# Optimization experiments

Hardware: AMD Instinct MI355X
Metric: run time of the kernel (lower is better)

Reference implementation:

```python
import jax, jax.numpy as jnp
import numpy as np

DIM, NH, WS, SS = 192, 6, 8, 4
B, H, W = 4, 192, 192
MID = max(DIM // 16, 4)
N = WS * WS
HD = DIM // NH
SCALE = HD ** -0.5

def _rel_index():
    coords = np.stack(np.meshgrid(np.arange(WS), np.arange(WS), indexing='ij')).reshape(2, -1)
    rel = (coords[:, :, None] - coords[:, None, :]).transpose(1, 2, 0)
    rel[..., 0] += WS - 1
    rel[..., 1] += WS - 1
    rel[..., 0] *= 2 * WS - 1
    return rel.sum(-1)  # (N, N)

REL_IDX = jnp.asarray(_rel_index())

def _shift_mask():
    img = np.zeros((1, H, W, 1), np.float32)
    sl = (slice(0, -WS), slice(-WS, -SS), slice(-SS, None))
    cnt = 0
    for hs in sl:
        for ws_ in sl:
            img[:, hs, ws_, :] = cnt
            cnt += 1
    mw = img.reshape(1, H // WS, WS, W // WS, WS, 1).transpose(0, 1, 3, 2, 4, 5).reshape(-1, N)
    am = mw[:, None, :] - mw[:, :, None]
    return jnp.asarray(np.where(am != 0, -100.0, 0.0).astype(np.float32))  # (nW, N, N)

MASK = _shift_mask()

def _win_part(x):  # (B,H,W,C) -> (B*nW, N, C)
    Bb, Hh, Ww, C = x.shape
    x = x.reshape(Bb, Hh // WS, WS, Ww // WS, WS, C).transpose(0, 1, 3, 2, 4, 5)
    return x.reshape(-1, N, C)

def _win_rev(x, Bb):  # (B*nW, N, C) -> (B,H,W,C)
    x = x.reshape(Bb, H // WS, W // WS, WS, WS, -1).transpose(0, 1, 3, 2, 4, 5)
    return x.reshape(Bb, H, W, -1)

def _ln(x, g, b):
    mu = x.mean(-1, keepdims=True)
    var = ((x - mu) ** 2).mean(-1, keepdims=True)
    return (x - mu) * jax.lax.rsqrt(var + 1e-5) * g + b

def _conv(x, w, b, groups=1):
    y = jax.lax.conv_general_dilated(x, w, (1, 1), 'SAME',
        dimension_numbers=('NCHW', 'OIHW', 'NCHW'), feature_group_count=groups)
    return y + b[None, :, None, None]

def _gelu(x):
    return jax.nn.gelu(x, approximate=False)  # torch default GELU is exact erf


def setup_inputs() -> dict:
    key = jax.random.key(0)
    ks = jax.random.split(key, 12)
    s = 0.02
    return {
        'x': jax.random.normal(ks[0], (B, DIM, H, W), jnp.float32),
        'norm1_g': jnp.ones((DIM,), jnp.float32),
        'norm1_b': jnp.zeros((DIM,), jnp.float32),
        'qkv_w': jax.random.normal(ks[1], (3 * DIM, DIM), jnp.float32) * s,
        'qkv_b': jnp.zeros((3 * DIM,), jnp.float32),
        'rel_table': jax.random.normal(ks[2], ((2 * WS - 1) ** 2, NH), jnp.float32) * s,
        'norm2_g': jnp.ones((DIM,), jnp.float32),
        'norm2_b': jnp.zeros((DIM,), jnp.float32),
        'mlp_w1': jax.random.normal(ks[3], (4 * DIM, DIM), jnp.float32) * s,
        'mlp_b1': jnp.zeros((4 * DIM,), jnp.float32),
        'mlp_w2': jax.random.normal(ks[4], (DIM, 4 * DIM), jnp.float32) * s,
        'mlp_b2': jnp.zeros((DIM,), jnp.float32),
        'ca_c1_w': jax.random.normal(ks[5], (DIM, DIM, 3, 3), jnp.float32) * s,
        'ca_c1_b': jnp.zeros((DIM,), jnp.float32),
        'ca_c2_w': jax.random.normal(ks[6], (DIM, DIM, 3, 3), jnp.float32) * s,
        'ca_c2_b': jnp.zeros((DIM,), jnp.float32),
        'se_w1': jax.random.normal(ks[7], (MID, DIM), jnp.float32) * s,
        'se_b1': jnp.zeros((MID,), jnp.float32),
        'se_w2': jax.random.normal(ks[8], (DIM, MID), jnp.float32) * s,
        'se_b2': jnp.zeros((DIM,), jnp.float32),
        'gate_w': jax.random.normal(ks[9], (DIM, 1, 3, 3), jnp.float32) * s,
        'gate_b': jnp.zeros((DIM,), jnp.float32),
    }


def reference(x, norm1_g, norm1_b, qkv_w, qkv_b, rel_table, norm2_g, norm2_b,
              mlp_w1, mlp_b1, mlp_w2, mlp_b2, ca_c1_w, ca_c1_b, ca_c2_w, ca_c2_b,
              se_w1, se_b1, se_w2, se_b2, gate_w, gate_b):
    Bb = x.shape[0]
    shortcut = x
    xh = _ln(x.transpose(0, 2, 3, 1), norm1_g, norm1_b)  # (B,H,W,C)
    xh = jnp.roll(xh, (-SS, -SS), (1, 2))                # shifted windows
    xw = _win_part(xh)                                   # (B*nW, N, C)
    qkv = jnp.einsum('bnc,dc->bnd', xw, qkv_w) + qkv_b
    qkv = qkv.reshape(-1, N, 3, NH, HD).transpose(2, 0, 3, 1, 4)
    q, k, v = qkv[0], qkv[1], qkv[2]                     # (B_, NH, N, HD)
    attn = jnp.einsum('bhnd,bhmd->bhnm', q * SCALE, k)
    bias = rel_table[REL_IDX.reshape(-1)].reshape(N, N, NH).transpose(2, 0, 1)
    attn = attn + bias[None]
    nW = MASK.shape[0]
    attn = attn.reshape(Bb, nW, NH, N, N) + MASK[None, :, None]
    attn = jax.nn.softmax(attn.reshape(-1, NH, N, N), axis=-1)
    out = jnp.einsum('bhnm,bhmd->bhnd', attn, v).transpose(0, 2, 1, 3).reshape(-1, N, DIM)
    # NOTE: original forward never applies self.proj; faithfully omitted.
    xh = _win_rev(out, Bb)
    xh = jnp.roll(xh, (SS, SS), (1, 2))
    x = shortcut + xh.transpose(0, 3, 1, 2)
    x = x + _conv(x, gate_w, gate_b, groups=DIM)         # depthwise conv gate
    # channel attention (conv body + SE)
    res = x
    y = _conv(x, ca_c1_w, ca_c1_b)
    y = _gelu(y)
    y = _conv(y, ca_c2_w, ca_c2_b)
    p = y.mean((2, 3))                                   # global avg pool -> (B,C)
    wgt = jax.nn.sigmoid(jax.nn.relu(p @ se_w1.T + se_b1) @ se_w2.T + se_b2)
    x = y * wgt[:, :, None, None] + res
    # MLP
    res = x
    xh = _ln(x.transpose(0, 2, 3, 1), norm2_g, norm2_b)
    xh = _gelu(jnp.einsum('bhwc,dc->bhwd', xh, mlp_w1) + mlp_b1)
    xh = jnp.einsum('bhwd,cd->bhwc', xh, mlp_w2) + mlp_b2
    return res + xh.transpose(0, 3, 1, 2)
```

## Files before the change

### kernel.cpp

```cpp
#include <hip/hip_runtime.h>
#include <hip/hip_bf16.h>

#define NWIN 576
#define SP 36864
#define ATT_SCALE 0.17677669529663687f

typedef unsigned short u16;
typedef unsigned int u32;
typedef __attribute__((ext_vector_type(8))) __bf16 bf16x8;
typedef __attribute__((ext_vector_type(4))) float f32x4;

__device__ __forceinline__ float b2f(u16 u){ return __uint_as_float(((u32)u)<<16); }
__device__ __forceinline__ u16 f2b(float f){ u32 u = __float_as_uint(f); return (u16)((u + 0x7FFFu + ((u>>16)&1u)) >> 16); }
__device__ __forceinline__ float fast_rcp(float d){ float r; asm("v_rcp_f32 %0, %1" : "=v"(r) : "v"(d)); return r; }
__device__ __forceinline__ u32 cvtpk(float lo, float hi){ u32 r; asm("v_cvt_pk_bf16_f32 %0, %1, %2" : "=v"(r) : "v"(lo), "v"(hi)); return r; }
__device__ __forceinline__ float gelu_f(float v){
  float u = v*(1.5957691216f + 0.0713548163f*v*v);
  return v * fast_rcp(1.0f + __expf(-u));
}
__device__ __forceinline__ f32x4 mfma16(bf16x8 a, bf16x8 b, f32x4 c){
  return __builtin_amdgcn_mfma_f32_16x16x32_bf16(a, b, c, 0, 0, 0);
}

__global__ __launch_bounds__(256) void k_transpose(const float* __restrict__ x, u16* __restrict__ xn){
  __shared__ float tile[32][33];
  int blk = blockIdx.x;
  int b = blk / 6912; int rem = blk % 6912;
  int h = rem / 36; int rem2 = rem % 36;
  int wt = rem2 / 6, ct = rem2 % 6;
  int t = threadIdx.x;
  int lw = t & 31, g = t >> 5;
  for (int r = 0; r < 4; ++r){
    int cl = g + r*8;
    tile[cl][lw] = x[(((size_t)b*192 + ct*32 + cl)*192 + h)*192 + wt*32 + lw];
  }
  __syncthreads();
  for (int r = 0; r < 4; ++r){
    int wl = g + r*8;
    xn[(((size_t)b*192 + h)*192 + wt*32 + wl)*192 + ct*32 + lw] = f2b(tile[lw][wl]);
  }
}

__global__ __launch_bounds__(256) void k_prep_all(
    const float* __restrict__ c1w, const float* __restrict__ c2w,
    const float* __restrict__ qkv_w, const float* __restrict__ rel_table,
    const float* __restrict__ mlp_w1, const float* __restrict__ mlp_w2,
    u16* __restrict__ Wpk1, u16* __restrict__ Wpk2, u16* __restrict__ Qkvpk,
    float* __restrict__ biasT, u16* __restrict__ W1pk, u16* __restrict__ W2pk){
  int i = blockIdx.x*256 + threadIdx.x;
  if (i < 331776){
    int j = i & 7; int l = (i >> 3) & 63; int rem = i >> 9;
    int nt = rem % 12; int rem2 = rem / 12; int kc = rem2 % 6; int tap = rem2 / 6;
    int ci = kc*32 + ((l>>4)<<3) + j;
    int co = nt*16 + (l & 15);
    Wpk1[i] = f2b(c1w[(co*192 + ci)*9 + tap]);
    Wpk2[i] = f2b(c2w[(co*192 + ci)*9 + tap]);
    return;
  }
  i -= 331776;
  if (i < 110592){
    int j = i & 7; int l = (i >> 3) & 63; int rem = i >> 9;
    int kc = rem % 6; int nt = rem / 6;
    int row = nt*16 + (l & 15); int c = kc*32 + ((l>>4)<<3) + j;
    Qkvpk[i] = f2b(qkv_w[row*192 + c]);
    return;
  }
  i -= 110592;
  if (i < 24576){
    int q = i & 63; int k = (i>>6) & 63; int h = i >> 12;
    int di = (q>>3) - (k>>3) + 7; int dj = (q&7) - (k&7) + 7;
    biasT[i] = rel_table[(di*15 + dj)*6 + h];
    return;
  }
  i -= 24576;
  if (i < 147456){
    int j = i & 7; int l = (i >> 3) & 63; int rem = i >> 9;
    int kc = rem % 6; int nt = rem / 6;
    int ho = nt*16 + (l & 15); int ci = kc*32 + ((l>>4)<<3) + j;
    W1pk[i] = f2b(mlp_w1[ho*192 + ci]);
    return;
  }
  i -= 147456;
  if (i < 147456){
    int j = i & 7; int l = (i >> 3) & 63; int rem = i >> 9;
    int kc = rem % 24; int nt = rem / 24;
    int co = nt*16 + (l & 15); int ho = kc*32 + ((l>>4)<<3) + j;
    W2pk[i] = f2b(mlp_w2[co*768 + ho]);
  }
}

__global__ __launch_bounds__(768, 3) void k_attn(const float* __restrict__ x, const u16* __restrict__ xn, int use_xn,
    const float* __restrict__ g1, const float* __restrict__ be1,
    const u16* __restrict__ qkvpk, const float* __restrict__ qkv_b,
    const float* __restrict__ biasT, u16* __restrict__ x1)
{
  __shared__ u16 xw[12800];
  __shared__ u16 qs[6][64][40];
  __shared__ u16 ks[6][64][40];
  __shared__ u16 vt[6][32][72];
  __shared__ int ih[64], iw[64], rid[64];
  __shared__ float red[64][12], red2[64][12], mu[64], rsg[64];
  int blk = blockIdx.x, t = threadIdx.x;
  int b = blk / NWIN, wi = blk % NWIN, wy = wi / 24, wx = wi % 24;
  int wid = t >> 6, l = t & 63, l15 = l & 15, lg = l >> 4;
  if (t < 64){
    int i = t >> 3, j = t & 7;
    int gh = wy*8 + i, gw = wx*8 + j;
    int hf = gh + 4; if (hf >= 192) hf -= 192;
    int wf = gw + 4; if (wf >= 192) wf -= 192;
    ih[t] = hf; iw[t] = wf;
    int rh = (gh < 184) ? 0 : ((gh < 188) ? 1 : 2);
    int rw = (gw < 184) ? 0 : ((gw < 188) ? 1 : 2);
    rid[t] = rh*3 + rw;
  }
  __syncthreads();
  if (use_xn){
    for (int idx = t; idx < 1536; idx += 768){
      int n = idx / 24, q = idx % 24;
      *(uint4*)&xw[n*200 + q*8] =
        *(const uint4*)(xn + ((size_t)((b*192 + ih[n])*192 + iw[n]))*192 + q*8);
    }
  } else {
    for (int idx = t; idx < 12288; idx += 768){
      int n = idx & 63, c = idx >> 6;
      xw[n*200 + c] = f2b(x[(((size_t)b*192 + c)*192 + ih[n])*192 + iw[n]]);
    }
  }
  __syncthreads();
  { int n = t / 12, part = t % 12;
    float s = 0.f, s2 = 0.f;
    for (int c = part*16; c < part*16 + 16; ++c){ float v = b2f(xw[n*200 + c]); s += v; s2 += v*v; }
    red[n][part] = s; red2[n][part] = s2; }
  __syncthreads();
  if (t < 64){
    float s = 0.f, s2 = 0.f;
    #pragma unroll
    for (int p = 0; p < 12; ++p){ s += red[t][p]; s2 += red2[t][p]; }
    float m = s * (1.f/192.f);
    float v = s2 * (1.f/192.f) - m*m;
    mu[t] = m; rsg[t] = rsqrtf(v + 1e-5f);
  }
  __syncthreads();
  for (int idx = t; idx < 12288; idx += 768){
    int n = idx & 63, c = idx >> 6;
    float v = (b2f(xw[n*200 + c]) - mu[n]) * rsg[n] * g1[c] + be1[c];
    xw[n*200 + c] = f2b(v);
  }
  __syncthreads();
  {
    f32x4 acc[3][4];
    #pragma unroll
    for (int i3 = 0; i3 < 3; ++i3)
      #pragma unroll
      for (int mt = 0; mt < 4; ++mt) acc[i3][mt] = (f32x4){0.f,0.f,0.f,0.f};
    #pragma unroll
    for (int kc = 0; kc < 6; ++kc){
      bf16x8 a4[4];
      #pragma unroll
      for (int mt = 0; mt < 4; ++mt)
        a4[mt] = *(const bf16x8*)&xw[(mt*16 + l15)*200 + kc*32 + lg*8];
      #pragma unroll
      for (int i3 = 0; i3 < 3; ++i3){
        int ntg = wid*3 + i3;
        bf16x8 bf = *(const bf16x8*)(qkvpk + ((size_t)ntg*6 + kc)*512 + l*8);
        #pragma unroll
        for (int mt = 0; mt < 4; ++mt)
          acc[i3][mt] = mfma16(a4[mt], bf, acc[i3][mt]);
      }
    }
    #pragma unroll
    for (int i3 = 0; i3 < 3; ++i3){
      int ntg = wid*3 + i3;
      float bv = qkv_b[ntg*16 + l15];
      int m = ntg/12, hh = (ntg%12)>>1, hd0 = (ntg&1)*16;
      #pragma unroll
      for (int mt = 0; mt < 4; ++mt)
        #pragma unroll
        for (int r = 0; r < 4; ++r){
          int tok = mt*16 + lg*4 + r;
          float val = acc[i3][mt][r] + bv;
          if (m == 0){ qs[hh][tok][hd0 + l15] = f2b(val * ATT_SCALE); }
          else if (m == 1){ ks[hh][tok][hd0 + l15] = f2b(val); }
          else { vt[hh][hd0 + l15][tok] = f2b(val); }
        }
    }
  }
  __syncthreads();
  int h = wid >> 1, mt0 = (wid & 1) * 2;
  f32x4 st[2][4];
  {
    bf16x8 bq0 = *(const bf16x8*)&qs[h][(mt0  )*16 + l15][lg*8];
    bf16x8 bq1 = *(const bf16x8*)&qs[h][(mt0+1)*16 + l15][lg*8];
    #pragma unroll
    for (int nt = 0; nt < 4; ++nt){
      bf16x8 ak = *(const bf16x8*)&ks[h][nt*16 + l15][lg*8];
      st[0][nt] = mfma16(ak, bq0, (f32x4){0.f,0.f,0.f,0.f});
      st[1][nt] = mfma16(ak, bq1, (f32x4){0.f,0.f,0.f,0.f});
    }
  }
  u32 pk[2][4][2];
  #pragma unroll
  for (int m2 = 0; m2 < 2; ++m2){
    int qg = (mt0 + m2)*16 + l15;
    int rq = rid[qg];
    const float* bp = biasT + (size_t)h*4096 + qg;
    float mx = -1e30f;
    #pragma unroll
    for (int nt = 0; nt < 4; ++nt)
      #pragma unroll
      for (int r = 0; r < 4; ++r){
        int kg = nt*16 + lg*4 + r;
        float v = st[m2][nt][r] + bp[kg*64] + (rq != rid[kg] ? -100.f : 0.f);
        st[m2][nt][r] = v;
        mx = fmaxf(mx, v);
      }
    mx = fmaxf(mx, __shfl_xor(mx, 16));
    mx = fmaxf(mx, __shfl_xor(mx, 32));
    float ssum = 0.f;
    #pragma unroll
    for (int nt = 0; nt < 4; ++nt)
      #pragma unroll
      for (int r = 0; r < 4; ++r){
        float e = __expf(st[m2][nt][r] - mx);
        st[m2][nt][r] = e; ssum += e;
      }
    ssum += __shfl_xor(ssum, 16);
    ssum += __shfl_xor(ssum, 32);
    float inv = fast_rcp(ssum);
    #pragma unroll
    for (int nt = 0; nt < 4; ++nt){
      pk[m2][nt][0] = cvtpk(st[m2][nt][0]*inv, st[m2][nt][1]*inv);
      pk[m2][nt][1] = cvtpk(st[m2][nt][2]*inv, st[m2][nt][3]*inv);
    }
  }
  f32x4 o[2][2];
  #pragma unroll
  for (int m2 = 0; m2 < 2; ++m2)
    #pragma unroll
    for (int nd = 0; nd < 2; ++nd) o[m2][nd] = (f32x4){0.f,0.f,0.f,0.f};
  {
    int srcA = ((lg & 1) << 1)*16 + l15;
    bool hiSel = (lg & 2) != 0;
    #pragma unroll
    for (int kc = 0; kc < 2; ++kc){
      bf16x8 bv0 = *(const bf16x8*)&vt[h][l15][kc*32 + lg*8];
      bf16x8 bv1 = *(const bf16x8*)&vt[h][16 + l15][kc*32 + lg*8];
      #pragma unroll
      for (int m2 = 0; m2 < 2; ++m2){
        u32 q0 = __shfl((int)pk[m2][2*kc  ][0], srcA);
        u32 q1 = __shfl((int)pk[m2][2*kc+1][0], srcA);
        u32 q2 = __shfl((int)pk[m2][2*kc  ][1], srcA);
        u32 q3 = __shfl((int)pk[m2][2*kc+1][1], srcA);
        u32 q4 = __shfl((int)pk[m2][2*kc  ][0], srcA + 16);
        u32 q5 = __shfl((int)pk[m2][2*kc+1][0], srcA + 16);
        u32 q6 = __shfl((int)pk[m2][2*kc  ][1], srcA + 16);
        u32 q7 = __shfl((int)pk[m2][2*kc+1][1], srcA + 16);
        union { u32 u[4]; bf16x8 v; } ap;
        ap.u[0] = hiSel ? q1 : q0;
        ap.u[1] = hiSel ? q3 : q2;
        ap.u[2] = hiSel ? q5 : q4;
        ap.u[3] = hiSel ? q7 : q6;
        o[m2][0] = mfma16(ap.v, bv0, o[m2][0]);
        o[m2][1] = mfma16(ap.v, bv1, o[m2][1]);
      }
    }
  }
  #pragma unroll
  for (int m2 = 0; m2 < 2; ++m2)
    #pragma unroll
    for (int nd = 0; nd < 2; ++nd)
      #pragma unroll
      for (int r = 0; r < 4; ++r){
        int tok = (mt0 + m2)*16 + lg*4 + r;
        xw[tok*200 + h*32 + nd*16 + l15] = f2b(o[m2][nd][r]);
      }
  __syncthreads();
  if (use_xn){
    for (int idx = t; idx < 1536; idx += 768){
      int n = idx / 24, q = idx % 24;
      size_t tokoff = (size_t)((b*192 + ih[n])*192 + iw[n]);
      uint4 xv = *(const uint4*)(xn + tokoff*192 + q*8);
      uint4 ov = *(const uint4*)&xw[n*200 + q*8];
      uint4 res;
      u32* xp = (u32*)&xv; u32* op = (u32*)&ov; u32* rp = (u32*)&res;
      #pragma unroll
      for (int w2 = 0; w2 < 4; ++w2){
        float a0 = b2f((u16)(xp[w2] & 0xffffu)) + b2f((u16)(op[w2] & 0xffffu));
        float a1 = b2f((u16)(xp[w2] >> 16))    + b2f((u16)(op[w2] >> 16));
        rp[w2] = (u32)f2b(a0) | ((u32)f2b(a1) << 16);
      }
      *(uint4*)(x1 + tokoff*192 + q*8) = res;
    }
  } else {
    for (int idx = t; idx < 12288; idx += 768){
      int n = idx & 63, c = idx >> 6;
      size_t tokoff = (size_t)((b*192 + ih[n])*192 + iw[n]);
      float sc = x[(((size_t)b*192 + c)*192 + ih[n])*192 + iw[n]];
      x1[tokoff*192 + c] = f2b(sc + b2f(xw[n*200 + c]));
    }
  }
}

__global__ __launch_bounds__(192) void k_gate(const u16* __restrict__ x1, const float* __restrict__ gw,
                                              const float* __restrict__ gb, u16* __restrict__ x2){
  int bid = blockIdx.x;
  int blk = (bid & 7) * 2304 + (bid >> 3);
  int wt = blk % 24; int rem = blk / 24;
  int h = rem % 192; int b = rem / 192;
  int c = threadIdx.x;
  int w0 = wt*8;
  float wr[9];
  #pragma unroll
  for (int p = 0; p < 9; ++p) wr[p] = gw[c*9 + p];
  float bias = gb[c];
  float in[3][10];
  #pragma unroll
  for (int dy = 0; dy < 3; ++dy){
    int hh = h + dy - 1;
    bool hok = (hh >= 0 && hh < 192);
    #pragma unroll
    for (int p = 0; p < 10; ++p){
      int ww = w0 + p - 1;
      bool ok = hok && (ww >= 0 && ww < 192);
      in[dy][p] = ok ? b2f(x1[(((size_t)b*192 + hh)*192 + ww)*192 + c]) : 0.f;
    }
  }
  size_t rowbase = ((size_t)b*192 + h)*192;
  #pragma unroll
  for (int i = 0; i < 8; ++i){
    float acc = bias;
    #pragma unroll
    for (int dy = 0; dy < 3; ++dy)
      #pragma unroll
      for (int dx = 0; dx < 3; ++dx)
        acc += in[dy][i + dx] * wr[dy*3 + dx];
    float v = in[1][i + 1] + acc;
    x2[(rowbase + w0 + i)*192 + c] = f2b(v);
  }
}

__global__ __launch_bounds__(256) void k_conv(const u16* __restrict__ src, const u16* __restrict__ wpk,
                                              const float* __restrict__ cb, u16* __restrict__ dst, int do_gelu){
  __shared__ u16 tin[20592];
  int bid = blockIdx.x;
  int blk = (bid & 7) * 288 + (bid >> 3);
  int b = blk / 576; int rem = blk % 576;
  int h = rem / 3; int w0 = (rem % 3) * 64;
  int t = threadIdx.x;
  int wid = t >> 6, l = t & 63;
  int l15 = l & 15, lg = l >> 4;
  f32x4 acc[4][3];
  #pragma unroll
  for (int mt = 0; mt < 4; ++mt)
    #pragma unroll
    for (int j = 0; j < 3; ++j) acc[mt][j] = (f32x4){0.f,0.f,0.f,0.f};
  for (int ch = 0; ch < 2; ++ch){
    __syncthreads();
    for (int idx = t; idx < 2376; idx += 256){
      int r = idx / 792; int r2 = idx % 792; int p = r2 / 12; int q = r2 % 12;
      int hh = h + r - 1, ww = w0 + p - 1;
      uint4 v = make_uint4(0u,0u,0u,0u);
      if (hh >= 0 && hh < 192 && ww >= 0 && ww < 192)
        v = *(const uint4*)(src + (((size_t)(b*192 + hh))*192 + ww)*192 + ch*96 + q*8);
      *(uint4*)&tin[(r*66 + p)*104 + q*8] = v;
    }
    __syncthreads();
    for (int dy = 0; dy < 3; ++dy){
      for (int kch = 0; kch < 3; ++kch){
        bf16x8 af[4][3];
        #pragma unroll
        for (int mt = 0; mt < 4; ++mt)
          #pragma unroll
          for (int dx = 0; dx < 3; ++dx)
            af[mt][dx] = *(const bf16x8*)&tin[(dy*66 + mt*16 + l15 + dx)*104 + kch*32 + lg*8];
        bf16x8 bw[3][3];
        int kc = ch*3 + kch;
        #pragma unroll
        for (int dx = 0; dx < 3; ++dx)
          #pragma unroll
          for (int j = 0; j < 3; ++j)
            bw[dx][j] = *(const bf16x8*)(wpk + ((((size_t)(dy*3+dx)*6 + kc)*12 + wid*3 + j)*64 + l)*8);
        __builtin_amdgcn_s_setprio(1);
        #pragma unroll
        for (int dx = 0; dx < 3; ++dx)
          #pragma unroll
          for (int j = 0; j < 3; ++j)
            #pragma unroll
            for (int mt = 0; mt < 4; ++mt)
              acc[mt][j] = mfma16(af[mt][dx], bw[dx][j], acc[mt][j]);
        __builtin_amdgcn_s_setprio(0);
      }
    }
  }
  __syncthreads();
  float bv[3];
  #pragma unroll
  for (int j = 0; j < 3; ++j) bv[j] = cb[wid*48 + j*16 + l15];
  #pragma unroll
  for (int mt = 0; mt < 4; ++mt)
    #pragma unroll
    for (int j = 0; j < 3; ++j)
      #pragma unroll
      for (int r = 0; r < 4; ++r){
        int pix = mt*16 + lg*4 + r;
        float v = acc[mt][j][r] + bv[j];
        if (do_gelu) v = gelu_f(v);
        tin[pix*200 + wid*48 + j*16 + l15] = f2b(v);
      }
  __syncthreads();
  for (int idx = t; idx < 1536; idx += 256){
    int pix = idx / 24, q = idx % 24;
    *(uint4*)(dst + (((size_t)(b*192 + h))*192 + w0 + pix)*192 + q*8) = *(const uint4*)&tin[pix*200 + q*8];
  }
}

__global__ __launch_bounds__(192) void k_pool(const u16* __restrict__ y2, float* __restrict__ pp){
  int blk = blockIdx.x; int b = blk / 36, ch = blk % 36;
  int c = threadIdx.x;
  float s = 0.f;
  for (int tok = ch*1024; tok < ch*1024 + 1024; ++tok)
    s += b2f(y2[((size_t)b*SP + tok)*192 + c]);
  pp[((size_t)b*36 + ch)*192 + c] = s;
}

__global__ __launch_bounds__(256) void k_se(const float* __restrict__ pp, const float* __restrict__ w1,
    const float* __restrict__ bb1, const float* __restrict__ w2, const float* __restrict__ bb2,
    float* __restrict__ wgt){
  __shared__ float pb[192]; __shared__ float hq[12];
  int t = threadIdx.x;
  for (int b = 0; b < 4; ++b){
    if (t < 192){ float s = 0.f; for (int ch = 0; ch < 36; ++ch) s += pp[((size_t)b*36 + ch)*192 + t]; pb[t] = s * (1.f/36864.f); }
    __syncthreads();
    if (t < 12){ float a = bb1[t]; for (int c = 0; c < 192; ++c) a += pb[c]*w1[t*192 + c]; hq[t] = fmaxf(a, 0.f); }
    __syncthreads();
    if (t < 192){ float a = bb2[t]; for (int m = 0; m < 12; ++m) a += hq[m]*w2[t*12 + m]; wgt[b*192 + t] = 1.f/(1.f + __expf(-a)); }
    __syncthreads();
  }
}

__global__ __launch_bounds__(256) void k_combine(const u16* __restrict__ y2, const u16* __restrict__ x2,
                                                 const float* __restrict__ wgt, u16* __restrict__ x3){
  size_t e = ((size_t)blockIdx.x*256 + threadIdx.x)*4;
  int c = (int)(e % 192);
  int b = (int)(e / ((size_t)SP*192));
  uint2 ya = *(const uint2*)(y2 + e);
  uint2 xa = *(const uint2*)(x2 + e);
  float4 wf = *(const float4*)(wgt + b*192 + c);
  float r0 = b2f((u16)(ya.x & 0xffffu))*wf.x + b2f((u16)(xa.x & 0xffffu));
  float r1 = b2f((u16)(ya.x >> 16))   *wf.y + b2f((u16)(xa.x >> 16));
  float r2 = b2f((u16)(ya.y & 0xffffu))*wf.z + b2f((u16)(xa.y & 0xffffu));
  float r3 = b2f((u16)(ya.y >> 16))   *wf.w + b2f((u16)(xa.y >> 16));
  uint2 o; o.x = (u32)f2b(r0) | ((u32)f2b(r1)<<16); o.y = (u32)f2b(r2) | ((u32)f2b(r3)<<16);
  *(uint2*)(x3 + e) = o;
}

__global__ __launch_bounds__(256, 2) void k_mlp(const u16* __restrict__ src0, const u16* __restrict__ src1,
    const float* __restrict__ wgt, int fused, const u16* __restrict__ W1pk,
    const float* __restrict__ mb1, const u16* __restrict__ W2pk, const float* __restrict__ mb2,
    const float* __restrict__ g2, const float* __restrict__ bt2, float* __restrict__ out){
  __shared__ u16 lnS[32][200];
  __shared__ u16 hidH[32*384];
  __shared__ float mu[32], rsg[32];
  int blk = blockIdx.x, t = threadIdx.x;
  int b = blk / 1152; int rem = blk % 1152;
  int h = rem / 6; int w0 = (rem % 6) * 32;
  size_t tokbase = ((size_t)b*192 + h)*192 + w0;
  int wid = t >> 6, l = t & 63, l15 = l & 15, lg = l >> 4;
  char* hb = (char*)hidH;
  if (fused){
    for (int idx = t; idx < 768; idx += 256){
      int tok = idx / 24, q = idx % 24;
      uint4 yv = *(const uint4*)(src0 + (tokbase + tok)*192 + q*8);
      uint4 xv = *(const uint4*)(src1 + (tokbase + tok)*192 + q*8);
      const float* wb = wgt + b*192 + q*8;
      uint4 res;
      u32* yp = (u32*)&yv; u32* xp = (u32*)&xv; u32* rp = (u32*)&res;
      #pragma unroll
      for (int w2 = 0; w2 < 4; ++w2){
        float r0 = b2f((u16)(yp[w2] & 0xffffu))*wb[2*w2]   + b2f((u16)(xp[w2] & 0xffffu));
        float r1 = b2f((u16)(yp[w2] >> 16))   *wb[2*w2+1] + b2f((u16)(xp[w2] >> 16));
        rp[w2] = cvtpk(r0, r1);
      }
      *(uint4*)&lnS[tok][q*8] = res;
    }
  } else {
    for (int idx = t; idx < 768; idx += 256){
      int tok = idx / 24, q = idx % 24;
      *(uint4*)&lnS[tok][q*8] = *(const uint4*)(src0 + (tokbase + tok)*192 + q*8);
    }
  }
  __syncthreads();
  { int tok = t >> 3, part = t & 7;
    float s = 0.f, s2 = 0.f;
    #pragma unroll
    for (int i = 0; i < 3; ++i){
      uint4 v = *(const uint4*)&lnS[tok][part*8 + 64*i];
      u32* vp = (u32*)&v;
      #pragma unroll
      for (int q = 0; q < 4; ++q){
        float a = b2f((u16)(vp[q] & 0xffffu)), c2 = b2f((u16)(vp[q] >> 16));
        s += a + c2; s2 += a*a + c2*c2;
      }
    }
    #pragma unroll
    for (int d = 1; d < 8; d <<= 1){
      s  += __shfl_xor(s, d);
      s2 += __shfl_xor(s2, d);
    }
    if (part == 0){
      float m = s*(1.f/192.f); float v = s2*(1.f/192.f) - m*m;
      mu[tok] = m; rsg[tok] = rsqrtf(v + 1e-5f);
    } }
  __syncthreads();
  int nb = wid*3;
  float resv[2][3][4];
  #pragma unroll
  for (int mt = 0; mt < 2; ++mt)
    #pragma unroll
    for (int j = 0; j < 3; ++j)
      #pragma unroll
      for (int r = 0; r < 4; ++r)
        resv[mt][j][r] = b2f(lnS[mt*16 + lg*4 + r][(nb+j)*16 + l15]);
  __syncthreads();
  { u32* lw = (u32*)lnS;
    for (int idx = t; idx < 3072; idx += 256){
      int tok = idx / 96, cp = idx % 96;
      int c0 = cp*2;
      float v0 = (b2f(lnS[tok][c0])   - mu[tok]) * rsg[tok] * g2[c0]   + bt2[c0];
      float v1 = (b2f(lnS[tok][c0+1]) - mu[tok]) * rsg[tok] * g2[c0+1] + bt2[c0+1];
      lw[tok*100 + cp] = cvtpk(v0, v1);
    } }
  __syncthreads();
  bf16x8 bT[2][6];
  #pragma unroll
  for (int tt = 0; tt < 2; ++tt)
    #pragma unroll
    for (int kc = 0; kc < 6; ++kc)
      bT[tt][kc] = *(const bf16x8*)&lnS[tt*16 + l15][kc*32 + lg*8];
  f32x4 acc2[2][3];
  #pragma unroll
  for (int mt = 0; mt < 2; ++mt)
    #pragma unroll
    for (int j = 0; j < 3; ++j) acc2[mt][j] = (f32x4){0.f,0.f,0.f,0.f};
  #pragma unroll
  for (int ph = 0; ph < 2; ++ph){
    #pragma unroll
    for (int i = 0; i < 6; ++i){
      int hot = ph*24 + wid*6 + i;
      bf16x8 aw[6];
      #pragma unroll
      for (int kc = 0; kc < 6; ++kc)
        aw[kc] = *(const bf16x8*)(W1pk + ((size_t)(hot*6 + kc)*64 + l)*8);
      float4 b4 = *(const float4*)(mb1 + hot*16 + lg*4);
      int hoL = (wid*6 + i)*16 + lg*4;
      #pragma unroll
      for (int tt = 0; tt < 2; ++tt){
        f32x4 acc = (f32x4){0.f,0.f,0.f,0.f};
        __builtin_amdgcn_s_setprio(1);
        #pragma unroll
        for (int kc = 0; kc < 6; ++kc)
          acc = mfma16(aw[kc], bT[tt][kc], acc);
        __builtin_amdgcn_s_setprio(0);
        u32 p0 = cvtpk(gelu_f(acc[0] + b4.x), gelu_f(acc[1] + b4.y));
        u32 p1 = cvtpk(gelu_f(acc[2] + b4.z), gelu_f(acc[3] + b4.w));
        int tok = tt*16 + l15;
        int byt = (tok*768 + hoL*2) ^ ((l15 & 7) << 4);
        *(uint2*)(hb + byt) = make_uint2(p0, p1);
      }
    }
    __syncthreads();
    #pragma unroll 2
    for (int kc = 0; kc < 12; ++kc){
      int by0 = ((      l15)*768 + (kc*32 + lg*8)*2) ^ ((l15 & 7) << 4);
      int by1 = ((16 +  l15)*768 + (kc*32 + lg*8)*2) ^ ((l15 & 7) << 4);
      bf16x8 a0 = *(const bf16x8*)(hb + by0);
      bf16x8 a1 = *(const bf16x8*)(hb + by1);
      bf16x8 bw3[3];
      #pragma unroll
      for (int j = 0; j < 3; ++j)
        bw3[j] = *(const bf16x8*)(W2pk + (((size_t)(nb + j)*24 + ph*12 + kc)*64 + l)*8);
      __builtin_amdgcn_s_setprio(1);
      #pragma unroll
      for (int j = 0; j < 3; ++j){
        acc2[0][j] = mfma16(a0, bw3[j], acc2[0][j]);
        acc2[1][j] = mfma16(a1, bw3[j], acc2[1][j]);
      }
      __builtin_amdgcn_s_setprio(0);
    }
    __syncthreads();
  }
  #pragma unroll
  for (int j = 0; j < 3; ++j){
    int co = (nb + j)*16 + l15;
    float bj = mb2[co];
    #pragma unroll
    for (int mt = 0; mt < 2; ++mt){
      int tok0 = mt*16 + lg*4;
      float4 ov;
      #pragma unroll
      for (int r = 0; r < 4; ++r)
        ((float*)&ov)[r] = resv[mt][j][r] + acc2[mt][j][r] + bj;
      *(float4*)(out + (((size_t)b*192 + co)*192 + h)*192 + w0 + tok0) = ov;
    }
  }
}

extern "C" void kernel_launch(void* const* d_in, const int* in_sizes, int n_in,
                              void* d_out, int out_size, void* d_ws, size_t ws_size,
                              hipStream_t stream){
  const float* x      = (const float*)d_in[0];
  const float* n1g    = (const float*)d_in[1];
  const float* n1b    = (const float*)d_in[2];
  const float* qkv_w  = (const float*)d_in[3];
  const float* qkv_b  = (const float*)d_in[4];
  const float* rel_t  = (const float*)d_in[5];
  const float* n2g    = (const float*)d_in[6];
  const float* n2b    = (const float*)d_in[7];
  const float* mlp_w1 = (const float*)d_in[8];
  const float* mlp_b1 = (const float*)d_in[9];
  const float* mlp_w2 = (const float*)d_in[10];
  const float* mlp_b2 = (const float*)d_in[11];
  const float* c1w    = (const float*)d_in[12];
  const float* c1b    = (const float*)d_in[13];
  const float* c2w    = (const float*)d_in[14];
  const float* c2b    = (const float*)d_in[15];
  const float* sew1   = (const float*)d_in[16];
  const float* seb1   = (const float*)d_in[17];
  const float* sew2   = (const float*)d_in[18];
  const float* seb2   = (const float*)d_in[19];
  const float* gw     = (const float*)d_in[20];
  const float* gb     = (const float*)d_in[21];

  const size_t E  = (size_t)4*192*192*192;
  const size_t EB = E*2;
  const size_t SMALL = 663552*2 + 221184 + 98304 + 294912*2 + 110592 + 3072 + 65536;
  char* ws = (char*)d_ws;
  u16* ws0 = (u16*)(ws);
  u16* ws1 = (u16*)(ws + EB);
  size_t off = 2*EB;
  int use_xn = (ws_size >= 3*EB + SMALL) ? 1 : 0;
  u16* xn = nullptr;
  if (use_xn){ xn = (u16*)(ws + off); off += EB; }
  u16* Wpk1  = (u16*)(ws + off); off += 663552;
  u16* Wpk2  = (u16*)(ws + off); off += 663552;
  u16* Qkvpk = (u16*)(ws + off); off += 221184;
  float* biasT = (float*)(ws + off); off += 98304;
  u16* W1pk = (u16*)(ws + off); off += 294912;
  u16* W2pk = (u16*)(ws + off); off += 294912;
  float* pp  = (float*)(ws + off); off += (size_t)4*36*192*4;
  float* wgt = (float*)(ws + off); off += 768*4;

  if (use_xn) k_transpose<<<27648, 256, 0, stream>>>(x, xn);
  k_prep_all<<<2976, 256, 0, stream>>>(c1w, c2w, qkv_w, rel_t, mlp_w1, mlp_w2,
                                       Wpk1, Wpk2, Qkvpk, biasT, W1pk, W2pk);

  k_attn<<<2304, 768, 0, stream>>>(x, xn, use_xn, n1g, n1b, Qkvpk, qkv_b, biasT, ws0);
  k_gate<<<18432, 192, 0, stream>>>(ws0, gw, gb, ws1);
  k_conv<<<2304, 256, 0, stream>>>(ws1, Wpk1, c1b, ws0, 1);
  u16* y2 = use_xn ? xn : (u16*)d_out;
  k_conv<<<2304, 256, 0, stream>>>(ws0, Wpk2, c2b, y2, 0);
  k_pool<<<144, 192, 0, stream>>>(y2, pp);
  k_se<<<1, 256, 0, stream>>>(pp, sew1, seb1, sew2, seb2, wgt);
  if (use_xn){
    k_mlp<<<4608, 256, 0, stream>>>(y2, ws1, wgt, 1, W1pk, mlp_b1, W2pk, mlp_b2, n2g, n2b, (float*)d_out);
  } else {
    k_combine<<<27648, 256, 0, stream>>>((const u16*)d_out, ws1, wgt, ws0);
    k_mlp<<<4608, 256, 0, stream>>>(ws0, ws0, wgt, 0, W1pk, mlp_b1, W2pk, mlp_b2, n2g, n2b, (float*)d_out);
  }
}
```

Before: 651.4 us.

## Fuse global average pooling into second conv epilogue and parallelise SE

The second conv kernel now sums its output tile per channel from shared memory and writes per-block partial sums, which removes the separate pooling pass that re-read the full conv output. The SE kernel runs one block per batch image and reduces the 576 partials instead of looping over batches in a single block. The transpose kernel processes four rows per block to cut the block count, and the unroll factors in the MLP kernel loops are adjusted. This costs a larger partial-sum buffer and a somewhat longer SE reduction.

```diff
diff --git a/kernel.cpp b/kernel.cpp
--- a/kernel.cpp
+++ b/kernel.cpp
@@ -25,19 +25,23 @@
 __global__ __launch_bounds__(256) void k_transpose(const float* __restrict__ x, u16* __restrict__ xn){
   __shared__ float tile[32][33];
   int blk = blockIdx.x;
-  int b = blk / 6912; int rem = blk % 6912;
-  int h = rem / 36; int rem2 = rem % 36;
+  int b = blk / 1728; int rem = blk % 1728;
+  int hg = rem / 36; int rem2 = rem % 36;
   int wt = rem2 / 6, ct = rem2 % 6;
   int t = threadIdx.x;
   int lw = t & 31, g = t >> 5;
-  for (int r = 0; r < 4; ++r){
-    int cl = g + r*8;
-    tile[cl][lw] = x[(((size_t)b*192 + ct*32 + cl)*192 + h)*192 + wt*32 + lw];
-  }
-  __syncthreads();
-  for (int r = 0; r < 4; ++r){
-    int wl = g + r*8;
-    xn[(((size_t)b*192 + h)*192 + wt*32 + wl)*192 + ct*32 + lw] = f2b(tile[lw][wl]);
+  for (int r4 = 0; r4 < 4; ++r4){
+    int h = hg*4 + r4;
+    for (int r = 0; r < 4; ++r){
+      int cl = g + r*8;
+      tile[cl][lw] = x[(((size_t)b*192 + ct*32 + cl)*192 + h)*192 + wt*32 + lw];
+    }
+    __syncthreads();
+    for (int r = 0; r < 4; ++r){
+      int wl = g + r*8;
+      xn[(((size_t)b*192 + h)*192 + wt*32 + wl)*192 + ct*32 + lw] = f2b(tile[lw][wl]);
+    }
+    __syncthreads();
   }
 }
 
@@ -340,7 +344,8 @@
 }
 
 __global__ __launch_bounds__(256) void k_conv(const u16* __restrict__ src, const u16* __restrict__ wpk,
-                                              const float* __restrict__ cb, u16* __restrict__ dst, int do_gelu){
+                                              const float* __restrict__ cb, u16* __restrict__ dst,
+                                              int do_gelu, float* __restrict__ pp){
   __shared__ u16 tin[20592];
   int bid = blockIdx.x;
   int blk = (bid & 7) * 288 + (bid >> 3);
@@ -412,15 +417,14 @@
     int pix = idx / 24, q = idx % 24;
     *(uint4*)(dst + (((size_t)(b*192 + h))*192 + w0 + pix)*192 + q*8) = *(const uint4*)&tin[pix*200 + q*8];
   }
-}
-
-__global__ __launch_bounds__(192) void k_pool(const u16* __restrict__ y2, float* __restrict__ pp){
-  int blk = blockIdx.x; int b = blk / 36, ch = blk % 36;
-  int c = threadIdx.x;
-  float s = 0.f;
-  for (int tok = ch*1024; tok < ch*1024 + 1024; ++tok)
-    s += b2f(y2[((size_t)b*SP + tok)*192 + c]);
-  pp[((size_t)b*36 + ch)*192 + c] = s;
+  if (pp){
+    if (t < 192){
+      float s = 0.f;
+      #pragma unroll 8
+      for (int pix = 0; pix < 64; ++pix) s += b2f(tin[pix*200 + t]);
+      pp[(size_t)blk*192 + t] = s;
+    }
+  }
 }
 
 __global__ __launch_bounds__(256) void k_se(const float* __restrict__ pp, const float* __restrict__ w1,
@@ -428,14 +432,17 @@
     float* __restrict__ wgt){
   __shared__ float pb[192]; __shared__ float hq[12];
   int t = threadIdx.x;
-  for (int b = 0; b < 4; ++b){
-    if (t < 192){ float s = 0.f; for (int ch = 0; ch < 36; ++ch) s += pp[((size_t)b*36 + ch)*192 + t]; pb[t] = s * (1.f/36864.f); }
-    __syncthreads();
-    if (t < 12){ float a = bb1[t]; for (int c = 0; c < 192; ++c) a += pb[c]*w1[t*192 + c]; hq[t] = fmaxf(a, 0.f); }
-    __syncthreads();
-    if (t < 192){ float a = bb2[t]; for (int m = 0; m < 12; ++m) a += hq[m]*w2[t*12 + m]; wgt[b*192 + t] = 1.f/(1.f + __expf(-a)); }
-    __syncthreads();
-  }
+  int b = blockIdx.x;
+  if (t < 192){
+    float s = 0.f;
+    const float* base = pp + (size_t)b*576*192 + t;
+    for (int ch = 0; ch < 576; ++ch) s += base[ch*192];
+    pb[t] = s * (1.f/36864.f);
+  }
+  __syncthreads();
+  if (t < 12){ float a = bb1[t]; for (int c = 0; c < 192; ++c) a += pb[c]*w1[t*192 + c]; hq[t] = fmaxf(a, 0.f); }
+  __syncthreads();
+  if (t < 192){ float a = bb2[t]; for (int m = 0; m < 12; ++m) a += hq[m]*w2[t*12 + m]; wgt[b*192 + t] = 1.f/(1.f + __expf(-a)); }
 }
 
 __global__ __launch_bounds__(256) void k_combine(const u16* __restrict__ y2, const u16* __restrict__ x2,
@@ -544,7 +551,7 @@
     for (int j = 0; j < 3; ++j) acc2[mt][j] = (f32x4){0.f,0.f,0.f,0.f};
   #pragma unroll
   for (int ph = 0; ph < 2; ++ph){
-    #pragma unroll
+    #pragma unroll 2
     for (int i = 0; i < 6; ++i){
       int hot = ph*24 + wid*6 + i;
       bf16x8 aw[6];
@@ -569,7 +576,7 @@
       }
     }
     __syncthreads();
-    #pragma unroll 2
+    #pragma unroll 3
     for (int kc = 0; kc < 12; ++kc){
       int by0 = ((      l15)*768 + (kc*32 + lg*8)*2) ^ ((l15 & 7) << 4);
       int by1 = ((16 +  l15)*768 + (kc*32 + lg*8)*2) ^ ((l15 & 7) << 4);
@@ -633,7 +640,7 @@
 
   const size_t E  = (size_t)4*192*192*192;
   const size_t EB = E*2;
-  const size_t SMALL = 663552*2 + 221184 + 98304 + 294912*2 + 110592 + 3072 + 65536;
+  const size_t SMALL = 663552*2 + 221184 + 98304 + 294912*2 + 4*576*192*4 + 768*4 + 65536;
   char* ws = (char*)d_ws;
   u16* ws0 = (u16*)(ws);
   u16* ws1 = (u16*)(ws + EB);
@@ -647,20 +654,19 @@
   float* biasT = (float*)(ws + off); off += 98304;
   u16* W1pk = (u16*)(ws + off); off += 294912;
   u16* W2pk = (u16*)(ws + off); off += 294912;
-  float* pp  = (float*)(ws + off); off += (size_t)4*36*192*4;
+  float* pp  = (float*)(ws + off); off += (size_t)4*576*192*4;
   float* wgt = (float*)(ws + off); off += 768*4;
 
-  if (use_xn) k_transpose<<<27648, 256, 0, stream>>>(x, xn);
+  if (use_xn) k_transpose<<<6912, 256, 0, stream>>>(x, xn);
   k_prep_all<<<2976, 256, 0, stream>>>(c1w, c2w, qkv_w, rel_t, mlp_w1, mlp_w2,
                                        Wpk1, Wpk2, Qkvpk, biasT, W1pk, W2pk);
 
   k_attn<<<2304, 768, 0, stream>>>(x, xn, use_xn, n1g, n1b, Qkvpk, qkv_b, biasT, ws0);
   k_gate<<<18432, 192, 0, stream>>>(ws0, gw, gb, ws1);
-  k_conv<<<2304, 256, 0, stream>>>(ws1, Wpk1, c1b, ws0, 1);
+  k_conv<<<2304, 256, 0, stream>>>(ws1, Wpk1, c1b, ws0, 1, nullptr);
   u16* y2 = use_xn ? xn : (u16*)d_out;
-  k_conv<<<2304, 256, 0, stream>>>(ws0, Wpk2, c2b, y2, 0);
-  k_pool<<<144, 192, 0, stream>>>(y2, pp);
-  k_se<<<1, 256, 0, stream>>>(pp, sew1, seb1, sew2, seb2, wgt);
+  k_conv<<<2304, 256, 0, stream>>>(ws0, Wpk2, c2b, y2, 0, pp);
+  k_se<<<4, 256, 0, stream>>>(pp, sew1, seb1, sew2, seb2, wgt);
   if (use_xn){
     k_mlp<<<4608, 256, 0, stream>>>(y2, ws1, wgt, 1, W1pk, mlp_b1, W2pk, mlp_b2, n2g, n2b, (float*)d_out);
   } else {
```

Result: faster. 587.6 us (-9.8%).
